# Kernel tuning notes

Measured on AMD Instinct MI355X. Metric: run time of the kernel, lower is better.

The kernel has to match this reference:

```python
import jax, jax.numpy as jnp
import numpy as np

NF4_LUT = jnp.array([-1.0, -0.6961928009986877, -0.5250730514526367, -0.39491719007492065,
                     -0.28444138169288635, -0.18477343022823334, -0.08820830285549164, 0.0,
                     0.07107656449079514, 0.14263366162776947, 0.22430233657360077,
                     0.3203405737876892, 0.4407068192958832, 0.5905631184577942,
                     0.796090841293335, 1.0], dtype=jnp.float32)

BLOCK_SIZE = 64
OUT_FEATURES = 11008
IN_FEATURES = 4096


def dequantize_nf4(packed, absmax, out_shape):
    # packed: (O, I//2) int codes 0..255; absmax: (O, num_blocks)
    higher = packed // 16
    lower = packed % 16
    unpacked = jnp.stack([lower, higher], axis=-1).reshape(out_shape)  # (O, I)
    dequant = NF4_LUT[unpacked]  # LUT gather -> fp32 (O, I)
    O, I = out_shape
    # block-wise absmax scale
    dequant = (dequant.reshape(O, I // BLOCK_SIZE, BLOCK_SIZE) * absmax[:, :, None]).reshape(O, I)
    return dequant


def setup_inputs() -> dict:
    key = jax.random.key(0)
    k1, k2, k3, k4 = jax.random.split(key, 4)
    x = jax.random.normal(k1, (4, 2048, IN_FEATURES), dtype=jnp.float32)
    weight = jax.random.randint(k2, (OUT_FEATURES, IN_FEATURES // 2), 0, 256, dtype=jnp.int32)
    absmax = jax.random.uniform(k3, (OUT_FEATURES, IN_FEATURES // BLOCK_SIZE), dtype=jnp.float32)
    bias = jax.random.normal(k4, (OUT_FEATURES,), dtype=jnp.float32)
    return {"x": x, "weight": weight, "absmax": absmax, "bias": bias}


def reference(x, weight, absmax, bias):
    w = dequantize_nf4(weight, absmax, (OUT_FEATURES, IN_FEATURES))  # (O, I)
    # F.linear: y = x @ w.T + bias
    return jnp.einsum('bsi,oi->bso', x, w) + bias
```

## Files before the change

kernel.cpp:

```cpp
#include <hip/hip_runtime.h>

#define IN_F 4096
#define OUT_F 11008

typedef __attribute__((ext_vector_type(8))) short bf16x8;
typedef __attribute__((ext_vector_type(4))) float f32x4;
typedef __attribute__((ext_vector_type(4))) unsigned short us4;
typedef __attribute__((ext_vector_type(8))) unsigned short us8;

__device__ __forceinline__ unsigned short f2bf(float f) {
  unsigned int u = __float_as_uint(f);
  u += 0x7FFFu + ((u >> 16) & 1u);
  return (unsigned short)(u >> 16);
}

__global__ __launch_bounds__(256) void prepass(const float* __restrict__ X,
                                               unsigned short* __restrict__ Xb, int n8,
                                               const int* __restrict__ Wp,
                                               const float* __restrict__ Amax,
                                               unsigned short* __restrict__ Wb, int n4,
                                               int xblk) {
  __shared__ float lutS[16];
  if (threadIdx.x < 16) {
    const float lut[16] = {-1.0f, -0.6961928009986877f, -0.5250730514526367f,
        -0.39491719007492065f, -0.28444138169288635f, -0.18477343022823334f,
        -0.08820830285549164f, 0.0f, 0.07107656449079514f, 0.14263366162776947f,
        0.22430233657360077f, 0.3203405737876892f, 0.4407068192958832f,
        0.5905631184577942f, 0.796090841293335f, 1.0f};
    lutS[threadIdx.x] = lut[threadIdx.x];
  }
  __syncthreads();
  if ((int)blockIdx.x < xblk) {
    for (int i = blockIdx.x * blockDim.x + threadIdx.x; i < n8;
         i += xblk * blockDim.x) {
      const float4 a = reinterpret_cast<const float4*>(X)[2 * i];
      const float4 b = reinterpret_cast<const float4*>(X)[2 * i + 1];
      us8 h;
      h[0] = f2bf(a.x); h[1] = f2bf(a.y); h[2] = f2bf(a.z); h[3] = f2bf(a.w);
      h[4] = f2bf(b.x); h[5] = f2bf(b.y); h[6] = f2bf(b.z); h[7] = f2bf(b.w);
      reinterpret_cast<us8*>(Xb)[i] = h;
    }
  } else {
    const int wgrid = gridDim.x - xblk;
    for (int i = (blockIdx.x - xblk) * blockDim.x + threadIdx.x; i < n4;
         i += wgrid * blockDim.x) {
      const int j = i * 4;
      const int row = j >> 11;
      const int coli = j & 2047;
      const float am = Amax[row * (IN_F / 64) + (coli >> 5)];
      const int4 pk = reinterpret_cast<const int4*>(Wp)[i];
      us8 h; int c;
      c = pk.x & 255; h[0] = f2bf(lutS[c & 15] * am); h[1] = f2bf(lutS[c >> 4] * am);
      c = pk.y & 255; h[2] = f2bf(lutS[c & 15] * am); h[3] = f2bf(lutS[c >> 4] * am);
      c = pk.z & 255; h[4] = f2bf(lutS[c & 15] * am); h[5] = f2bf(lutS[c >> 4] * am);
      c = pk.w & 255; h[6] = f2bf(lutS[c & 15] * am); h[7] = f2bf(lutS[c >> 4] * am);
      reinterpret_cast<us8*>(Wb)[i] = h;
    }
  }
}

#define MF(a, b, c) __builtin_amdgcn_mfma_f32_16x16x32_bf16(a, b, c, 0, 0, 0)
#define GLDS(src, dst) __builtin_amdgcn_global_load_lds( \
    (const __attribute__((address_space(1))) void*)(src), \
    (__attribute__((address_space(3))) void*)(dst), 16, 0, 0)
#define BAR __builtin_amdgcn_s_barrier()
#define VM2 asm volatile("s_waitcnt vmcnt(2)")
#define VM0 asm volatile("s_waitcnt vmcnt(0)")
#define P1 __builtin_amdgcn_s_setprio(1)
#define P0 __builtin_amdgcn_s_setprio(0)

__global__ __launch_bounds__(1024, 4) void gemm256w16(
    const unsigned short* __restrict__ A,
    const unsigned short* __restrict__ B,
    const float* __restrict__ Bias, float* __restrict__ Out, int M) {
  extern __shared__ unsigned short sm[];
  char* const smc = (char*)sm;

  const int tid = threadIdx.x;
  const int l = tid & 63;
  const int wid = tid >> 6;

  const int Nb = OUT_F / 256;

  const int bps = 16 * Nb;
  const int pxc = bps >> 3;
  const int i6 = (int)blockIdx.x % bps;
  const int sup = (int)blockIdx.x / bps;
  const int kk = (i6 & 7) * pxc + (i6 >> 3);
  const int m0 = (sup * 16 + (kk & 15)) * 256;
  const int n0 = (kk >> 4) * 256;

  const int wm = (wid >> 2) * 64;
  const int wn = (wid & 3) * 64;

  const int lv = (l & 15) * 64 + (((l >> 4) ^ ((l >> 1) & 3)) * 16);
  const int aLane = (wid >> 2) * 4096 + lv;
  const int bLane = 16384 + (wid & 3) * 4096 + lv;

  const int rq = tid >> 2;
  const int cs = (tid & 3) ^ ((tid >> 3) & 3);
  const unsigned short* gAs = A + (size_t)(m0 + rq) * IN_F + cs * 8;
  const unsigned short* gBs = B + (size_t)(n0 + rq) * IN_F + cs * 8;

#define SA(t, sl) GLDS(gAs + (size_t)(t) * 32, sm + (sl) * 16384 + wid * 512)
#define SB(t, sl) GLDS(gBs + (size_t)(t) * 32, sm + (sl) * 16384 + 8192 + wid * 512)

  f32x4 acc[4][4];
#pragma unroll
  for (int i = 0; i < 4; ++i)
#pragma unroll
    for (int j = 0; j < 4; ++j) acc[i][j] = {0.f, 0.f, 0.f, 0.f};

#define KT(T, SL, STG, VMW) do { \
    VMW; \
    BAR; \
    const char* Sb = smc + (SL) * 32768; \
    bf16x8 a0, a1, a2, a3, b0, b1, b2, b3; \
    a0 = *(const bf16x8*)(Sb + aLane);        a1 = *(const bf16x8*)(Sb + aLane + 1024); \
    a2 = *(const bf16x8*)(Sb + aLane + 2048); a3 = *(const bf16x8*)(Sb + aLane + 3072); \
    b0 = *(const bf16x8*)(Sb + bLane);        b1 = *(const bf16x8*)(Sb + bLane + 1024); \
    b2 = *(const bf16x8*)(Sb + bLane + 2048); b3 = *(const bf16x8*)(Sb + bLane + 3072); \
    if (STG) SA((T) + 2, ((SL) + 2) % 3); \
    P1; \
    acc[0][0]=MF(a0,b0,acc[0][0]); acc[0][1]=MF(a0,b1,acc[0][1]); \
    acc[0][2]=MF(a0,b2,acc[0][2]); acc[0][3]=MF(a0,b3,acc[0][3]); \
    acc[1][0]=MF(a1,b0,acc[1][0]); acc[1][1]=MF(a1,b1,acc[1][1]); \
    acc[1][2]=MF(a1,b2,acc[1][2]); acc[1][3]=MF(a1,b3,acc[1][3]); \
    P0; \
    if (STG) SB((T) + 2, ((SL) + 2) % 3); \
    P1; \
    acc[2][0]=MF(a2,b0,acc[2][0]); acc[2][1]=MF(a2,b1,acc[2][1]); \
    acc[2][2]=MF(a2,b2,acc[2][2]); acc[2][3]=MF(a2,b3,acc[2][3]); \
    acc[3][0]=MF(a3,b0,acc[3][0]); acc[3][1]=MF(a3,b1,acc[3][1]); \
    acc[3][2]=MF(a3,b2,acc[3][2]); acc[3][3]=MF(a3,b3,acc[3][3]); \
    P0; \
  } while (0)

  SA(0, 0); SB(0, 0); SA(1, 1); SB(1, 1);

  for (int T = 0; T < 126; T += 3) {
    KT(T, 0, (T < 124), VM2);
    KT(T + 1, 1, (T + 1 < 126), VM2);
    KT(T + 2, 2, (T + 2 < 126), VM2);
  }
  KT(126, 0, 0, VM2);
  KT(127, 1, 0, VM0);

  const int crow0 = m0 + wm + ((l >> 4) << 2);
  const int ccol0 = n0 + wn + (l & 15);
#pragma unroll
  for (int j = 0; j < 4; ++j) {
    const float bv = Bias[ccol0 + j * 16];
#pragma unroll
    for (int i = 0; i < 4; ++i)
#pragma unroll
      for (int rg = 0; rg < 4; ++rg)
        Out[(size_t)(crow0 + i * 16 + rg) * OUT_F + ccol0 + j * 16] = acc[i][j][rg] + bv;
  }
}

__global__ __launch_bounds__(256, 2) void nf4_gemm_fused(
    const float* __restrict__ X, const int* __restrict__ Wp,
    const float* __restrict__ Amax, const float* __restrict__ Bias,
    float* __restrict__ Out, int M) {
  __shared__ unsigned short As[128 * 64];
  __shared__ unsigned short Bs[128 * 64];
  __shared__ float lutS[16];

  const int t = threadIdx.x;
  const int l = t & 63;
  const int wid = t >> 6;

  if (t < 16) {
    const float lut[16] = {-1.0f, -0.6961928009986877f, -0.5250730514526367f,
        -0.39491719007492065f, -0.28444138169288635f, -0.18477343022823334f,
        -0.08820830285549164f, 0.0f, 0.07107656449079514f, 0.14263366162776947f,
        0.22430233657360077f, 0.3203405737876892f, 0.4407068192958832f,
        0.5905631184577942f, 0.796090841293335f, 1.0f};
    lutS[t] = lut[t];
  }

  const int ntile = OUT_F / 128;
  const int m0 = (blockIdx.x / ntile) * 128;
  const int n0 = (blockIdx.x % ntile) * 128;

  const int ar = t >> 4;
  const int ac4 = t & 15;
  const int br = t >> 3;
  const int bg = t & 7;
  const int wm = (wid >> 1) * 64;
  const int wn = (wid & 1) * 64;

  f32x4 acc[4][4];
#pragma unroll
  for (int i = 0; i < 4; ++i)
#pragma unroll
    for (int j = 0; j < 4; ++j) acc[i][j] = {0.f, 0.f, 0.f, 0.f};

  __syncthreads();

  for (int k0 = 0; k0 < IN_F; k0 += 64) {
#pragma unroll
    for (int p = 0; p < 8; ++p) {
      const int r = p * 16 + ar;
      const float4 v = *reinterpret_cast<const float4*>(
          X + (size_t)(m0 + r) * IN_F + k0 + ac4 * 4);
      us4 h;
      h[0] = f2bf(v.x); h[1] = f2bf(v.y); h[2] = f2bf(v.z); h[3] = f2bf(v.w);
      const int byte = r * 128 + ((ac4 * 8) ^ ((r & 7) << 4));
      *reinterpret_cast<us4*>(reinterpret_cast<char*>(As) + byte) = h;
    }
#pragma unroll
    for (int p = 0; p < 4; ++p) {
      const int r = p * 32 + br;
      const float amv = Amax[(size_t)(n0 + r) * (IN_F / 64) + (k0 >> 6)];
      const int4 pk = *reinterpret_cast<const int4*>(
          Wp + (size_t)(n0 + r) * (IN_F / 2) + (k0 >> 1) + bg * 4);
      us8 h;
      {
        int c;
        c = pk.x & 255; h[0] = f2bf(lutS[c & 15] * amv); h[1] = f2bf(lutS[c >> 4] * amv);
        c = pk.y & 255; h[2] = f2bf(lutS[c & 15] * amv); h[3] = f2bf(lutS[c >> 4] * amv);
        c = pk.z & 255; h[4] = f2bf(lutS[c & 15] * amv); h[5] = f2bf(lutS[c >> 4] * amv);
        c = pk.w & 255; h[6] = f2bf(lutS[c & 15] * amv); h[7] = f2bf(lutS[c >> 4] * amv);
      }
      const int byte = r * 128 + ((bg * 16) ^ ((r & 7) << 4));
      *reinterpret_cast<us8*>(reinterpret_cast<char*>(Bs) + byte) = h;
    }
    __syncthreads();

#pragma unroll
    for (int kkk = 0; kkk < 64; kkk += 32) {
      bf16x8 af[4], bfv[4];
      const int kb = (kkk + ((l >> 4) << 3)) * 2;
#pragma unroll
      for (int i = 0; i < 4; ++i) {
        const int row = wm + i * 16 + (l & 15);
        af[i] = *reinterpret_cast<const bf16x8*>(
            reinterpret_cast<const char*>(As) + row * 128 + (kb ^ ((row & 7) << 4)));
      }
#pragma unroll
      for (int j = 0; j < 4; ++j) {
        const int row = wn + j * 16 + (l & 15);
        bfv[j] = *reinterpret_cast<const bf16x8*>(
            reinterpret_cast<const char*>(Bs) + row * 128 + (kb ^ ((row & 7) << 4)));
      }
#pragma unroll
      for (int i = 0; i < 4; ++i)
#pragma unroll
        for (int j = 0; j < 4; ++j)
          acc[i][j] = __builtin_amdgcn_mfma_f32_16x16x32_bf16(af[i], bfv[j], acc[i][j], 0, 0, 0);
    }
    __syncthreads();
  }

  const int crow0 = m0 + wm + ((l >> 4) << 2);
  const int ccol0 = n0 + wn + (l & 15);
#pragma unroll
  for (int j = 0; j < 4; ++j) {
    const float bv = Bias[ccol0 + j * 16];
#pragma unroll
    for (int i = 0; i < 4; ++i)
#pragma unroll
      for (int rg = 0; rg < 4; ++rg)
        Out[(size_t)(crow0 + i * 16 + rg) * OUT_F + ccol0 + j * 16] = acc[i][j][rg] + bv;
  }
}

extern "C" void kernel_launch(void* const* d_in, const int* in_sizes, int n_in,
                              void* d_out, int out_size, void* d_ws, size_t ws_size,
                              hipStream_t stream) {
  const float* X = (const float*)d_in[0];
  const int* Wp = (const int*)d_in[1];
  const float* Amax = (const float*)d_in[2];
  const float* Bias = (const float*)d_in[3];
  float* Out = (float*)d_out;

  const int M = in_sizes[0] / IN_F;
  const size_t needX = (size_t)M * IN_F * 2;
  const size_t needW = (size_t)OUT_F * IN_F * 2;
  const int grid256 = (M / 256) * (OUT_F / 256);

  if (ws_size >= needX + needW && (M % 4096) == 0) {
    unsigned short* Xb = (unsigned short*)d_ws;
    unsigned short* Wb = Xb + (size_t)M * IN_F;
    (void)hipFuncSetAttribute(reinterpret_cast<const void*>(gemm256w16),
                              hipFuncAttributeMaxDynamicSharedMemorySize, 98304);
    prepass<<<4096, 256, 0, stream>>>(X, Xb, M * (IN_F / 8),
                                      Wp, Amax, Wb, OUT_F * (IN_F / 8), 2048);
    gemm256w16<<<grid256, 1024, 98304, stream>>>(Xb, Wb, Bias, Out, M);
  } else {
    const int grid = (M / 128) * (OUT_F / 128);
    nf4_gemm_fused<<<grid, 256, 0, stream>>>(X, Wp, Amax, Bias, Out, M);
  }
}
```

Baseline: 754.1 us.

## Switch GEMM to double-buffered K=64 tiles with full vmcnt wait

```diff
diff --git a/kernel.cpp b/kernel.cpp
--- a/kernel.cpp
+++ b/kernel.cpp
@@ -64,7 +64,6 @@
     (const __attribute__((address_space(1))) void*)(src), \
     (__attribute__((address_space(3))) void*)(dst), 16, 0, 0)
 #define BAR __builtin_amdgcn_s_barrier()
-#define VM2 asm volatile("s_waitcnt vmcnt(2)")
 #define VM0 asm volatile("s_waitcnt vmcnt(0)")
 #define P1 __builtin_amdgcn_s_setprio(1)
 #define P0 __builtin_amdgcn_s_setprio(0)
@@ -95,15 +94,17 @@
 
   const int lv = (l & 15) * 64 + (((l >> 4) ^ ((l >> 1) & 3)) * 16);
   const int aLane = (wid >> 2) * 4096 + lv;
-  const int bLane = 16384 + (wid & 3) * 4096 + lv;
+  const int bLane = 32768 + (wid & 3) * 4096 + lv;
 
   const int rq = tid >> 2;
   const int cs = (tid & 3) ^ ((tid >> 3) & 3);
   const unsigned short* gAs = A + (size_t)(m0 + rq) * IN_F + cs * 8;
   const unsigned short* gBs = B + (size_t)(n0 + rq) * IN_F + cs * 8;
 
-#define SA(t, sl) GLDS(gAs + (size_t)(t) * 32, sm + (sl) * 16384 + wid * 512)
-#define SB(t, sl) GLDS(gBs + (size_t)(t) * 32, sm + (sl) * 16384 + 8192 + wid * 512)
+#define SA(t, kh) GLDS(gAs + (size_t)(t) * 64 + (kh) * 32, \
+                       sm + ((t) & 1) * 32768 + (kh) * 8192 + wid * 512)
+#define SB(t, kh) GLDS(gBs + (size_t)(t) * 64 + (kh) * 32, \
+                       sm + ((t) & 1) * 32768 + 16384 + (kh) * 8192 + wid * 512)
 
   f32x4 acc[4][4];
 #pragma unroll
@@ -111,40 +112,39 @@
 #pragma unroll
     for (int j = 0; j < 4; ++j) acc[i][j] = {0.f, 0.f, 0.f, 0.f};
 
-#define KT(T, SL, STG, VMW) do { \
-    VMW; \
+#define MM16(A0, A1, A2, A3, B0, B1, B2, B3) do { \
+    acc[0][0]=MF(A0,B0,acc[0][0]); acc[0][1]=MF(A0,B1,acc[0][1]); \
+    acc[0][2]=MF(A0,B2,acc[0][2]); acc[0][3]=MF(A0,B3,acc[0][3]); \
+    acc[1][0]=MF(A1,B0,acc[1][0]); acc[1][1]=MF(A1,B1,acc[1][1]); \
+    acc[1][2]=MF(A1,B2,acc[1][2]); acc[1][3]=MF(A1,B3,acc[1][3]); \
+    acc[2][0]=MF(A2,B0,acc[2][0]); acc[2][1]=MF(A2,B1,acc[2][1]); \
+    acc[2][2]=MF(A2,B2,acc[2][2]); acc[2][3]=MF(A2,B3,acc[2][3]); \
+    acc[3][0]=MF(A3,B0,acc[3][0]); acc[3][1]=MF(A3,B1,acc[3][1]); \
+    acc[3][2]=MF(A3,B2,acc[3][2]); acc[3][3]=MF(A3,B3,acc[3][3]); } while (0)
+
+#define KT(T, STG) do { \
+    VM0; \
     BAR; \
-    const char* Sb = smc + (SL) * 32768; \
+    const char* Sb = smc + ((T) & 1) * 65536; \
     bf16x8 a0, a1, a2, a3, b0, b1, b2, b3; \
     a0 = *(const bf16x8*)(Sb + aLane);        a1 = *(const bf16x8*)(Sb + aLane + 1024); \
     a2 = *(const bf16x8*)(Sb + aLane + 2048); a3 = *(const bf16x8*)(Sb + aLane + 3072); \
     b0 = *(const bf16x8*)(Sb + bLane);        b1 = *(const bf16x8*)(Sb + bLane + 1024); \
     b2 = *(const bf16x8*)(Sb + bLane + 2048); b3 = *(const bf16x8*)(Sb + bLane + 3072); \
-    if (STG) SA((T) + 2, ((SL) + 2) % 3); \
-    P1; \
-    acc[0][0]=MF(a0,b0,acc[0][0]); acc[0][1]=MF(a0,b1,acc[0][1]); \
-    acc[0][2]=MF(a0,b2,acc[0][2]); acc[0][3]=MF(a0,b3,acc[0][3]); \
-    acc[1][0]=MF(a1,b0,acc[1][0]); acc[1][1]=MF(a1,b1,acc[1][1]); \
-    acc[1][2]=MF(a1,b2,acc[1][2]); acc[1][3]=MF(a1,b3,acc[1][3]); \
-    P0; \
-    if (STG) SB((T) + 2, ((SL) + 2) % 3); \
-    P1; \
-    acc[2][0]=MF(a2,b0,acc[2][0]); acc[2][1]=MF(a2,b1,acc[2][1]); \
-    acc[2][2]=MF(a2,b2,acc[2][2]); acc[2][3]=MF(a2,b3,acc[2][3]); \
-    acc[3][0]=MF(a3,b0,acc[3][0]); acc[3][1]=MF(a3,b1,acc[3][1]); \
-    acc[3][2]=MF(a3,b2,acc[3][2]); acc[3][3]=MF(a3,b3,acc[3][3]); \
-    P0; \
+    if (STG) { SA((T) + 1, 0); SA((T) + 1, 1); } \
+    P1; MM16(a0, a1, a2, a3, b0, b1, b2, b3); P0; \
+    a0 = *(const bf16x8*)(Sb + 16384 + aLane);        a1 = *(const bf16x8*)(Sb + 16384 + aLane + 1024); \
+    a2 = *(const bf16x8*)(Sb + 16384 + aLane + 2048); a3 = *(const bf16x8*)(Sb + 16384 + aLane + 3072); \
+    b0 = *(const bf16x8*)(Sb + 16384 + bLane);        b1 = *(const bf16x8*)(Sb + 16384 + bLane + 1024); \
+    b2 = *(const bf16x8*)(Sb + 16384 + bLane + 2048); b3 = *(const bf16x8*)(Sb + 16384 + bLane + 3072); \
+    if (STG) { SB((T) + 1, 0); SB((T) + 1, 1); } \
+    P1; MM16(a0, a1, a2, a3, b0, b1, b2, b3); P0; \
   } while (0)
 
-  SA(0, 0); SB(0, 0); SA(1, 1); SB(1, 1);
-
-  for (int T = 0; T < 126; T += 3) {
-    KT(T, 0, (T < 124), VM2);
-    KT(T + 1, 1, (T + 1 < 126), VM2);
-    KT(T + 2, 2, (T + 2 < 126), VM2);
-  }
-  KT(126, 0, 0, VM2);
-  KT(127, 1, 0, VM0);
+  SA(0, 0); SA(0, 1); SB(0, 0); SB(0, 1);
+
+  for (int T = 0; T < 63; ++T) { KT(T, 1); }
+  KT(63, 0);
 
   const int crow0 = m0 + wm + ((l >> 4) << 2);
   const int ccol0 = n0 + wn + (l & 15);
@@ -285,10 +285,10 @@
     unsigned short* Xb = (unsigned short*)d_ws;
     unsigned short* Wb = Xb + (size_t)M * IN_F;
     (void)hipFuncSetAttribute(reinterpret_cast<const void*>(gemm256w16),
-                              hipFuncAttributeMaxDynamicSharedMemorySize, 98304);
+                              hipFuncAttributeMaxDynamicSharedMemorySize, 131072);
     prepass<<<4096, 256, 0, stream>>>(X, Xb, M * (IN_F / 8),
                                       Wp, Amax, Wb, OUT_F * (IN_F / 8), 2048);
-    gemm256w16<<<grid256, 1024, 98304, stream>>>(Xb, Wb, Bias, Out, M);
+    gemm256w16<<<grid256, 1024, 131072, stream>>>(Xb, Wb, Bias, Out, M);
   } else {
     const int grid = (M / 128) * (OUT_F / 128);
     nf4_gemm_fused<<<grid, 256, 0, stream>>>(X, Wp, Amax, Bias, Out, M);
```

After: 776.3 us. 1.03x slower.
